# Kernel tuning notes

Measured on AMD Instinct MI355X. Metric: run time of the kernel, lower is better.

## Reference

```python
import jax, jax.numpy as jnp
import numpy as np

B, S, D, H = 4, 2048, 1024, 16
DH = D // H  # 64


def setup_inputs() -> dict:
    key = jax.random.key(0)
    ks = jax.random.split(key, 9)
    s_in = 1.0 / np.sqrt(D)
    inp = {
        "x_input": jax.random.normal(ks[0], (B, S, D), dtype=jnp.float32),
        # torch nn.Linear weights are [out, in]; y = x @ W.T + b
        "wq": jax.random.normal(ks[1], (D, D), dtype=jnp.float32) * s_in,
        "bq": jax.random.normal(ks[2], (D,), dtype=jnp.float32) * 0.01,
        "wk": jax.random.normal(ks[3], (D, D), dtype=jnp.float32) * s_in,
        "bk": jax.random.normal(ks[4], (D,), dtype=jnp.float32) * 0.01,
        "wv": jax.random.normal(ks[5], (D, D), dtype=jnp.float32) * s_in,
        "bv": jax.random.normal(ks[6], (D,), dtype=jnp.float32) * 0.01,
        "wo": jax.random.normal(ks[7], (D, D), dtype=jnp.float32) * s_in,
        "bo": jax.random.normal(ks[8], (D,), dtype=jnp.float32) * 0.01,
    }
    return inp


def reference(x_input, wq, bq, wk, bk, wv, bv, wo, bo):
    scale = 1.0 / np.sqrt(DH)
    q = x_input @ wq.T + bq  # [B,S,D]
    k = x_input @ wk.T + bk
    v = x_input @ wv.T + bv
    # split heads: [B,S,H,DH]
    q = q.reshape(B, S, H, DH)
    k = k.reshape(B, S, H, DH)
    v = v.reshape(B, S, H, DH)
    # scores [B,H,Sq,Sk] (vectorized over heads; same math as per-head loop)
    scores = jnp.einsum('bqhd,bkhd->bhqk', q, k) * scale
    attn = jax.nn.softmax(scores, axis=-1)
    out = jnp.einsum('bhqk,bkhd->bqhd', attn, v).reshape(B, S, D)
    return out @ wo.T + bo
```

## Files before the change

kernel.cpp:

```cpp
#include <hip/hip_runtime.h>

typedef unsigned short u16;
typedef unsigned int u32;
typedef unsigned int u32x2 __attribute__((ext_vector_type(2)));
typedef short bf16x8 __attribute__((ext_vector_type(8)));
typedef float f32x2 __attribute__((ext_vector_type(2)));
typedef float f32x4 __attribute__((ext_vector_type(4)));
typedef float f32x16 __attribute__((ext_vector_type(16)));

__device__ __forceinline__ u16 f2bf(float f) {
  unsigned int u = __builtin_bit_cast(unsigned int, f);
  u += 0x7FFFu + ((u >> 16) & 1u);
  return (u16)(u >> 16);
}

__device__ __forceinline__ u32 cvtpk(float lo, float hi) {
  u32 r;
  asm("v_cvt_pk_bf16_f32 %0, %1, %2" : "=v"(r) : "v"(lo), "v"(hi));
  return r;
}

#if __has_builtin(__builtin_amdgcn_exp2f)
#define EX2(x) __builtin_amdgcn_exp2f(x)
#else
extern "C" __device__ float __ocml_native_exp2_f32(float);
#define EX2(x) __ocml_native_exp2_f32(x)
#endif

#define MFMA16(a, b, c) __builtin_amdgcn_mfma_f32_16x16x32_bf16((a), (b), (c), 0, 0, 0)
#define MFMA32(a, b, c) __builtin_amdgcn_mfma_f32_32x32x16_bf16((a), (b), (c), 0, 0, 0)

#define GLL16(gp, lp) __builtin_amdgcn_global_load_lds( \
    (const __attribute__((address_space(1))) unsigned int*)(gp), \
    (__attribute__((address_space(3))) unsigned int*)(lp), 16, 0, 0)

__global__ __launch_bounds__(256) void cvt_bf16(const float* __restrict__ in,
                                                u16* __restrict__ out, int n4) {
  int i = blockIdx.x * 256 + threadIdx.x;
  const int stride = gridDim.x * 256;
  for (; i < n4; i += stride) {
    float4 f = ((const float4*)in)[i];
    u32x2 o;
    o[0] = cvtpk(f.x, f.y);
    o[1] = cvtpk(f.z, f.w);
    ((u32x2*)out)[i] = o;
  }
}

__global__ __launch_bounds__(256) void cvt_w4(const float* __restrict__ w0,
                                              const float* __restrict__ w1,
                                              const float* __restrict__ w2,
                                              const float* __restrict__ w3,
                                              u16* __restrict__ out) {
  const int wsel = blockIdx.y;
  const float* in = wsel == 0 ? w0 : wsel == 1 ? w1 : wsel == 2 ? w2 : w3;
  const int i = blockIdx.x * 256 + threadIdx.x;
  float4 f = ((const float4*)in)[i];
  u32x2 o;
  o[0] = cvtpk(f.x, f.y);
  o[1] = cvtpk(f.z, f.w);
  ((u32x2*)(out + (size_t)wsel * 1048576))[i] = o;
}

__global__ __launch_bounds__(256) void gemm_qkv(const u16* __restrict__ A,
                                                const u16* __restrict__ W,
                                                const float* __restrict__ bq,
                                                const float* __restrict__ bk,
                                                const float* __restrict__ bv,
                                                float qscale,
                                                u16* __restrict__ Qo,
                                                u16* __restrict__ Ko,
                                                u16* __restrict__ Vo) {
  __shared__ u16 As[128 * 64];
  __shared__ u16 Bs[128 * 64];
  const int t = threadIdx.x;
  const int wave = t >> 6, lane = t & 63;
  const int wg = blockIdx.x;
  const int s = (wg & 7) * 192 + (wg >> 3);
  const int bx = s & 63, by = s >> 6;
  const int bm = bx * 128, bn3 = by * 128;
  const int wr = (wave >> 1) * 64;
  const int wc = (wave & 1) * 64;
  f32x4 acc[4][4] = {};

  const u16* Ag[4];
  const u16* Bg[4];
#pragma unroll
  for (int i = 0; i < 4; i++) {
    const int c = i * 256 + t;
    const int row = c >> 3;
    const int g8 = (((c & 7) ^ (row & 7)) << 3);
    Ag[i] = A + (size_t)(bm + row) * 1024 + g8;
    Bg[i] = W + (size_t)(bn3 + row) * 1024 + g8;
  }

  const int frow = lane & 15;
  const int l4 = lane >> 4;

  for (int k0 = 0; k0 < 1024; k0 += 64) {
#pragma unroll
    for (int i = 0; i < 4; i++) GLL16(Ag[i], &As[i * 2048 + wave * 512]);
#pragma unroll
    for (int i = 0; i < 4; i++) GLL16(Bg[i], &Bs[i * 2048 + wave * 512]);
    __syncthreads();
    bf16x8 a[4][2], b[4][2];
#pragma unroll
    for (int m = 0; m < 4; m++) {
      const int row = wr + m * 16 + frow, sw = row & 7;
      a[m][0] = *(const bf16x8*)&As[row * 64 + ((l4 ^ sw) << 3)];
      a[m][1] = *(const bf16x8*)&As[row * 64 + (((l4 + 4) ^ sw) << 3)];
    }
#pragma unroll
    for (int n = 0; n < 4; n++) {
      const int row = wc + n * 16 + frow, sw = row & 7;
      b[n][0] = *(const bf16x8*)&Bs[row * 64 + ((l4 ^ sw) << 3)];
      b[n][1] = *(const bf16x8*)&Bs[row * 64 + (((l4 + 4) ^ sw) << 3)];
    }
#pragma unroll
    for (int m = 0; m < 4; m++)
#pragma unroll
      for (int n = 0; n < 4; n++) {
        acc[m][n] = MFMA16(a[m][0], b[n][0], acc[m][n]);
        acc[m][n] = MFMA16(a[m][1], b[n][1], acc[m][n]);
      }
    __syncthreads();
#pragma unroll
    for (int i = 0; i < 4; i++) { Ag[i] += 64; Bg[i] += 64; }
  }

  const int mode = by >> 3;
  const float* bias = mode == 0 ? bq : mode == 1 ? bk : bv;
  u16* out = mode == 0 ? Qo : Ko;
  const float alpha = mode == 0 ? qscale : 1.0f;

  const int crow0 = bm + wr + ((lane >> 4) << 2);
  const int ccolb = (bn3 & 1023) + wc + frow;
#pragma unroll
  for (int n = 0; n < 4; n++) {
    const int col = ccolb + n * 16;
    const float bvv = bias[col];
#pragma unroll
    for (int m = 0; m < 4; m++) {
      if (mode == 2) {
        const int row = crow0 + m * 16;
        u32x2 w;
        w[0] = cvtpk(acc[m][n][0] + bvv, acc[m][n][1] + bvv);
        w[1] = cvtpk(acc[m][n][2] + bvv, acc[m][n][3] + bvv);
        size_t off = ((size_t)((row >> 11) * 16 + (col >> 6)) * 64 + (col & 63)) * 2048 + (row & 2047);
        *(u32x2*)(Vo + off) = w;
      } else {
#pragma unroll
        for (int r = 0; r < 4; r++) {
          float v = (acc[m][n][r] + bvv) * alpha;
          out[(size_t)(crow0 + m * 16 + r) * 1024 + col] = f2bf(v);
        }
      }
    }
  }
}

__global__ __launch_bounds__(256) void gemm_out(const u16* __restrict__ A,
                                                const u16* __restrict__ W,
                                                const float* __restrict__ bias,
                                                float* __restrict__ C) {
  __shared__ u16 As[128 * 64];
  __shared__ u16 Bs[128 * 64];
  const int t = threadIdx.x;
  const int wave = t >> 6, lane = t & 63;
  const int wg = blockIdx.x;
  const int s = (wg & 7) * 64 + (wg >> 3);
  const int bx = s & 63, by = s >> 6;
  const int bm = bx * 128, bn = by * 128;
  const int wr = (wave >> 1) * 64;
  const int wc = (wave & 1) * 64;
  f32x4 acc[4][4] = {};

  const u16* Ag[4];
  const u16* Bg[4];
#pragma unroll
  for (int i = 0; i < 4; i++) {
    const int c = i * 256 + t;
    const int row = c >> 3;
    const int g8 = (((c & 7) ^ (row & 7)) << 3);
    Ag[i] = A + (size_t)(bm + row) * 1024 + g8;
    Bg[i] = W + (size_t)(bn + row) * 1024 + g8;
  }

  const int frow = lane & 15;
  const int l4 = lane >> 4;

  for (int k0 = 0; k0 < 1024; k0 += 64) {
#pragma unroll
    for (int i = 0; i < 4; i++) GLL16(Ag[i], &As[i * 2048 + wave * 512]);
#pragma unroll
    for (int i = 0; i < 4; i++) GLL16(Bg[i], &Bs[i * 2048 + wave * 512]);
    __syncthreads();
    bf16x8 a[4][2], b[4][2];
#pragma unroll
    for (int m = 0; m < 4; m++) {
      const int row = wr + m * 16 + frow, sw = row & 7;
      a[m][0] = *(const bf16x8*)&As[row * 64 + ((l4 ^ sw) << 3)];
      a[m][1] = *(const bf16x8*)&As[row * 64 + (((l4 + 4) ^ sw) << 3)];
    }
#pragma unroll
    for (int n = 0; n < 4; n++) {
      const int row = wc + n * 16 + frow, sw = row & 7;
      b[n][0] = *(const bf16x8*)&Bs[row * 64 + ((l4 ^ sw) << 3)];
      b[n][1] = *(const bf16x8*)&Bs[row * 64 + (((l4 + 4) ^ sw) << 3)];
    }
#pragma unroll
    for (int m = 0; m < 4; m++)
#pragma unroll
      for (int n = 0; n < 4; n++) {
        acc[m][n] = MFMA16(a[m][0], b[n][0], acc[m][n]);
        acc[m][n] = MFMA16(a[m][1], b[n][1], acc[m][n]);
      }
    __syncthreads();
#pragma unroll
    for (int i = 0; i < 4; i++) { Ag[i] += 64; Bg[i] += 64; }
  }

  const int crow0 = bm + wr + ((lane >> 4) << 2);
  const int ccol = bn + wc + frow;
#pragma unroll
  for (int n = 0; n < 4; n++) {
    float bvv = bias[ccol + n * 16];
#pragma unroll
    for (int m = 0; m < 4; m++)
#pragma unroll
      for (int r = 0; r < 4; r++)
        C[(size_t)(crow0 + m * 16 + r) * 1024 + (ccol + n * 16)] = acc[m][n][r] + bvv;
  }
}

__global__ __launch_bounds__(256, 4) void attn2(const u16* __restrict__ Q,
                                                const u16* __restrict__ K,
                                                const u16* __restrict__ VT,
                                                u16* __restrict__ O) {
  __shared__ u16 ks[2][4096];
  __shared__ u16 vs[4096];
  __shared__ u16 ps[4][2048];
  const int t = threadIdx.x;
  const int lane = t & 63, warp = t >> 6;
  const int g = lane >> 5, ql = lane & 31;
  const int wg = blockIdx.x;
  const int idx = wg >> 3;
  const int bh = ((wg & 7) << 3) + (idx >> 4);
  const int qblk = idx & 15;
  const int b = bh >> 4, h = bh & 15;

  bf16x8 qf[4];
  {
    const u16* qp = Q + (size_t)(b * 2048 + qblk * 128 + warp * 32 + ql) * 1024 + h * 64 + 8 * g;
#pragma unroll
    for (int kk = 0; kk < 4; kk++) qf[kk] = *(const bf16x8*)(qp + 16 * kk);
  }

  int offRC[2][4];
#pragma unroll
  for (int kk = 0; kk < 4; kk++) {
    int x = (((2 * kk + g) ^ (ql & 7)) << 3);
    offRC[0][kk] = ql * 64 + x;
    offRC[1][kk] = (32 + ql) * 64 + x;
  }

  const int c0 = t, c1 = t + 256;
  const int r0 = c0 >> 3, r1 = c1 >> 3;
  const u16* kp0 = K + (size_t)(b * 2048 + r0) * 1024 + h * 64 + (((c0 & 7) ^ (r0 & 7)) << 3);
  const u16* kp1 = K + (size_t)(b * 2048 + r1) * 1024 + h * 64 + (((c1 & 7) ^ (r1 & 7)) << 3);
  const u16* vp0 = VT + ((size_t)bh * 64 + r0) * 2048 + (((c0 & 7) ^ (r0 & 7)) << 3);
  const u16* vp1 = VT + ((size_t)bh * 64 + r1) * 2048 + (((c1 & 7) ^ (r1 & 7)) << 3);
  const size_t kadv = (size_t)64 * 1024;

  f32x16 o0 = {}, o1 = {};
  float l = 0.f;

  GLL16(kp0, &ks[0][warp * 512]);
  GLL16(kp1, &ks[0][2048 + warp * 512]);
  kp0 += kadv; kp1 += kadv;
  __syncthreads();

  u16* pwq = &ps[warp][0] + ql * 64;
  const int sw = ql & 7;
  const int e4 = (((ql >> 3) ^ (ql >> 4)) & 1) << 2;

  int cur = 0;
  for (int kt = 0; kt < 32; kt++) {
    const int nxt = cur ^ 1;
    GLL16(vp0, &vs[warp * 512]);
    GLL16(vp1, &vs[2048 + warp * 512]);
    vp0 += 64; vp1 += 64;
    GLL16(kp0, &ks[nxt][warp * 512]);
    GLL16(kp1, &ks[nxt][2048 + warp * 512]);
    kp0 += kadv; kp1 += kadv;

    const u16* kb = ks[cur];

    f32x16 s0 = {}, s1 = {};
    __builtin_amdgcn_s_setprio(1);
#pragma unroll
    for (int kk = 0; kk < 4; kk++) {
      bf16x8 ka = *(const bf16x8*)(kb + offRC[0][kk]);
      bf16x8 kc = *(const bf16x8*)(kb + offRC[1][kk]);
      s0 = MFMA32(ka, qf[kk], s0);
      s1 = MFMA32(kc, qf[kk], s1);
    }
    __builtin_amdgcn_s_setprio(0);

    {
      f32x2* s0p = (f32x2*)&s0;
      f32x2* s1p = (f32x2*)&s1;
      f32x2 tsum[8];
#pragma unroll
      for (int i = 0; i < 8; i++) {
        f32x2 d0 = s0p[i], d1 = s1p[i];
        d0[0] = EX2(d0[0]); d0[1] = EX2(d0[1]);
        d1[0] = EX2(d1[0]); d1[1] = EX2(d1[1]);
        s0p[i] = d0; s1p[i] = d1;
        tsum[i] = d0 + d1;
      }
#pragma unroll
      for (int i = 0; i < 4; i++) tsum[i] += tsum[i + 4];
      tsum[0] += tsum[2]; tsum[1] += tsum[3];
      tsum[0] += tsum[1];
      l += tsum[0][0] + tsum[0][1];
    }

#pragma unroll
    for (int q4 = 0; q4 < 4; q4++) {
      u32x2 wa, wb;
      wa[0] = cvtpk(s0[4 * q4 + 0], s0[4 * q4 + 1]);
      wa[1] = cvtpk(s0[4 * q4 + 2], s0[4 * q4 + 3]);
      wb[0] = cvtpk(s1[4 * q4 + 0], s1[4 * q4 + 1]);
      wb[1] = cvtpk(s1[4 * q4 + 2], s1[4 * q4 + 3]);
      const int so = (g << 2) ^ e4;
      *(u32x2*)(pwq + ((q4 ^ sw) << 3) + so) = wa;
      *(u32x2*)(pwq + (((q4 + 4) ^ sw) << 3) + so) = wb;
    }
    asm volatile("s_waitcnt lgkmcnt(0)" ::: "memory");
    __builtin_amdgcn_sched_barrier(0);

    bf16x8 pf[4];
#pragma unroll
    for (int kg = 0; kg < 4; kg++) {
      const u16* gb = pwq + (((2 * kg + g) ^ sw) << 3);
      union { u32x2 w[2]; bf16x8 v; } u;
      u.w[0] = *(const u32x2*)(gb + e4);
      u.w[1] = *(const u32x2*)(gb + (e4 ^ 4));
      pf[kg] = u.v;
    }

    asm volatile("s_waitcnt vmcnt(2)" ::: "memory");
    __builtin_amdgcn_s_barrier();
    __builtin_amdgcn_sched_barrier(0);

    __builtin_amdgcn_s_setprio(1);
#pragma unroll
    for (int kg = 0; kg < 4; kg++) {
      bf16x8 va = *(const bf16x8*)(vs + offRC[0][kg]);
      bf16x8 vc = *(const bf16x8*)(vs + offRC[1][kg]);
      o0 = MFMA32(va, pf[kg], o0);
      o1 = MFMA32(vc, pf[kg], o1);
    }
    __builtin_amdgcn_s_setprio(0);

    asm volatile("s_waitcnt vmcnt(0)" ::: "memory");
    __builtin_amdgcn_s_barrier();
    __builtin_amdgcn_sched_barrier(0);
    cur = nxt;
  }

  l += __shfl_xor(l, 32);
  const float rinv = 1.0f / l;
  u16* op = O + (size_t)(b * 2048 + qblk * 128 + warp * 32 + ql) * 1024 + h * 64;
#pragma unroll
  for (int half = 0; half < 2; half++) {
    const f32x16& oo = half ? o1 : o0;
#pragma unroll
    for (int p = 0; p < 4; p++) {
      u32x2 w;
      w[0] = cvtpk(oo[4 * p + 0] * rinv, oo[4 * p + 1] * rinv);
      w[1] = cvtpk(oo[4 * p + 2] * rinv, oo[4 * p + 3] * rinv);
      const int dh = 8 * p + 4 * g + 32 * half;
      *(u32x2*)(op + dh) = w;
    }
  }
}

extern "C" void kernel_launch(void* const* d_in, const int* in_sizes, int n_in,
                              void* d_out, int out_size, void* d_ws, size_t ws_size,
                              hipStream_t stream) {
  const float* x  = (const float*)d_in[0];
  const float* wq = (const float*)d_in[1];
  const float* bq = (const float*)d_in[2];
  const float* wk = (const float*)d_in[3];
  const float* bk = (const float*)d_in[4];
  const float* wv = (const float*)d_in[5];
  const float* bv = (const float*)d_in[6];
  const float* wo = (const float*)d_in[7];
  const float* bo = (const float*)d_in[8];

  u16* xb  = (u16*)d_ws;
  u16* wqb = xb + 8388608;
  u16* wob = wqb + 3145728;
  u16* qb  = wob + 1048576;
  u16* kb  = qb + 8388608;
  u16* vtb = kb + 8388608;
  u16* ob  = xb;

  cvt_bf16<<<2048, 256, 0, stream>>>(x, xb, 8388608 / 4);
  cvt_w4<<<dim3(1024, 4), 256, 0, stream>>>(wq, wk, wv, wo, wqb);

  const float qscale = 0.125f * 1.44269504088896f;
  gemm_qkv<<<1536, 256, 0, stream>>>(xb, wqb, bq, bk, bv, qscale, qb, kb, vtb);

  attn2<<<1024, 256, 0, stream>>>(qb, kb, vtb, ob);

  gemm_out<<<512, 256, 0, stream>>>(ob, wob, bo, (float*)d_out);
}
```

Before: 206.0 us.

## Process two query sub-tiles per warp in attention to reuse K/V tiles

Each attention workgroup now handles 256 query rows instead of 128: every warp computes two 32-row query slices against the same K and V tiles held in shared memory. This halves the grid and halves the global K/V traffic and the LDS K/V reads per query row. In exchange it doubles the accumulator and fragment registers per thread, lowers the launch-bounds occupancy hint from 4 to 2, and leaves fewer workgroups to fill the GPU.

```diff
diff --git a/kernel.cpp b/kernel.cpp
--- a/kernel.cpp
+++ b/kernel.cpp
@@ -233,7 +233,7 @@
   }
 }
 
-__global__ __launch_bounds__(256, 4) void attn2(const u16* __restrict__ Q,
+__global__ __launch_bounds__(256, 2) void attn2(const u16* __restrict__ Q,
                                                 const u16* __restrict__ K,
                                                 const u16* __restrict__ VT,
                                                 u16* __restrict__ O) {
@@ -245,15 +245,16 @@
   const int g = lane >> 5, ql = lane & 31;
   const int wg = blockIdx.x;
   const int idx = wg >> 3;
-  const int bh = ((wg & 7) << 3) + (idx >> 4);
-  const int qblk = idx & 15;
+  const int bh = ((wg & 7) << 3) + (idx >> 3);
+  const int qblk = idx & 7;
   const int b = bh >> 4, h = bh & 15;
 
-  bf16x8 qf[4];
-  {
-    const u16* qp = Q + (size_t)(b * 2048 + qblk * 128 + warp * 32 + ql) * 1024 + h * 64 + 8 * g;
-#pragma unroll
-    for (int kk = 0; kk < 4; kk++) qf[kk] = *(const bf16x8*)(qp + 16 * kk);
+  bf16x8 qf[2][4];
+#pragma unroll
+  for (int s = 0; s < 2; s++) {
+    const u16* qp = Q + (size_t)(b * 2048 + qblk * 256 + warp * 64 + s * 32 + ql) * 1024 + h * 64 + 8 * g;
+#pragma unroll
+    for (int kk = 0; kk < 4; kk++) qf[s][kk] = *(const bf16x8*)(qp + 16 * kk);
   }
 
   int offRC[2][4];
@@ -272,8 +273,8 @@
   const u16* vp1 = VT + ((size_t)bh * 64 + r1) * 2048 + (((c1 & 7) ^ (r1 & 7)) << 3);
   const size_t kadv = (size_t)64 * 1024;
 
-  f32x16 o0 = {}, o1 = {};
-  float l = 0.f;
+  f32x16 oa0 = {}, oa1 = {}, ob0 = {}, ob1 = {};
+  float l0 = 0.f, l1 = 0.f;
 
   GLL16(kp0, &ks[0][warp * 512]);
   GLL16(kp1, &ks[0][2048 + warp * 512]);
@@ -283,6 +284,7 @@
   u16* pwq = &ps[warp][0] + ql * 64;
   const int sw = ql & 7;
   const int e4 = (((ql >> 3) ^ (ql >> 4)) & 1) << 2;
+  const int so = (g << 2) ^ e4;
 
   int cur = 0;
   for (int kt = 0; kt < 32; kt++) {
@@ -296,58 +298,69 @@
 
     const u16* kb = ks[cur];
 
-    f32x16 s0 = {}, s1 = {};
-    __builtin_amdgcn_s_setprio(1);
+    bf16x8 kf0[4], kf1[4];
 #pragma unroll
     for (int kk = 0; kk < 4; kk++) {
-      bf16x8 ka = *(const bf16x8*)(kb + offRC[0][kk]);
-      bf16x8 kc = *(const bf16x8*)(kb + offRC[1][kk]);
-      s0 = MFMA32(ka, qf[kk], s0);
-      s1 = MFMA32(kc, qf[kk], s1);
-    }
-    __builtin_amdgcn_s_setprio(0);
-
-    {
-      f32x2* s0p = (f32x2*)&s0;
-      f32x2* s1p = (f32x2*)&s1;
-      f32x2 tsum[8];
-#pragma unroll
-      for (int i = 0; i < 8; i++) {
-        f32x2 d0 = s0p[i], d1 = s1p[i];
-        d0[0] = EX2(d0[0]); d0[1] = EX2(d0[1]);
-        d1[0] = EX2(d1[0]); d1[1] = EX2(d1[1]);
-        s0p[i] = d0; s1p[i] = d1;
-        tsum[i] = d0 + d1;
-      }
-#pragma unroll
-      for (int i = 0; i < 4; i++) tsum[i] += tsum[i + 4];
-      tsum[0] += tsum[2]; tsum[1] += tsum[3];
-      tsum[0] += tsum[1];
-      l += tsum[0][0] + tsum[0][1];
-    }
-
-#pragma unroll
-    for (int q4 = 0; q4 < 4; q4++) {
-      u32x2 wa, wb;
-      wa[0] = cvtpk(s0[4 * q4 + 0], s0[4 * q4 + 1]);
-      wa[1] = cvtpk(s0[4 * q4 + 2], s0[4 * q4 + 3]);
-      wb[0] = cvtpk(s1[4 * q4 + 0], s1[4 * q4 + 1]);
-      wb[1] = cvtpk(s1[4 * q4 + 2], s1[4 * q4 + 3]);
-      const int so = (g << 2) ^ e4;
-      *(u32x2*)(pwq + ((q4 ^ sw) << 3) + so) = wa;
-      *(u32x2*)(pwq + (((q4 + 4) ^ sw) << 3) + so) = wb;
-    }
-    asm volatile("s_waitcnt lgkmcnt(0)" ::: "memory");
-    __builtin_amdgcn_sched_barrier(0);
-
-    bf16x8 pf[4];
-#pragma unroll
-    for (int kg = 0; kg < 4; kg++) {
-      const u16* gb = pwq + (((2 * kg + g) ^ sw) << 3);
-      union { u32x2 w[2]; bf16x8 v; } u;
-      u.w[0] = *(const u32x2*)(gb + e4);
-      u.w[1] = *(const u32x2*)(gb + (e4 ^ 4));
-      pf[kg] = u.v;
+      kf0[kk] = *(const bf16x8*)(kb + offRC[0][kk]);
+      kf1[kk] = *(const bf16x8*)(kb + offRC[1][kk]);
+    }
+
+    bf16x8 pf0[4], pf1[4];
+#pragma unroll
+    for (int s = 0; s < 2; s++) {
+      f32x16 s0 = {}, s1 = {};
+      __builtin_amdgcn_s_setprio(1);
+#pragma unroll
+      for (int kk = 0; kk < 4; kk++) {
+        s0 = MFMA32(kf0[kk], qf[s][kk], s0);
+        s1 = MFMA32(kf1[kk], qf[s][kk], s1);
+      }
+      __builtin_amdgcn_s_setprio(0);
+
+      {
+        f32x2* s0p = (f32x2*)&s0;
+        f32x2* s1p = (f32x2*)&s1;
+        f32x2 tsum[8];
+#pragma unroll
+        for (int i = 0; i < 8; i++) {
+          f32x2 d0 = s0p[i], d1 = s1p[i];
+          d0[0] = EX2(d0[0]); d0[1] = EX2(d0[1]);
+          d1[0] = EX2(d1[0]); d1[1] = EX2(d1[1]);
+          s0p[i] = d0; s1p[i] = d1;
+          tsum[i] = d0 + d1;
+        }
+#pragma unroll
+        for (int i = 0; i < 4; i++) tsum[i] += tsum[i + 4];
+        tsum[0] += tsum[2]; tsum[1] += tsum[3];
+        tsum[0] += tsum[1];
+        if (s == 0) l0 += tsum[0][0] + tsum[0][1];
+        else        l1 += tsum[0][0] + tsum[0][1];
+      }
+
+#pragma unroll
+      for (int q4 = 0; q4 < 4; q4++) {
+        u32x2 wa, wb;
+        wa[0] = cvtpk(s0[4 * q4 + 0], s0[4 * q4 + 1]);
+        wa[1] = cvtpk(s0[4 * q4 + 2], s0[4 * q4 + 3]);
+        wb[0] = cvtpk(s1[4 * q4 + 0], s1[4 * q4 + 1]);
+        wb[1] = cvtpk(s1[4 * q4 + 2], s1[4 * q4 + 3]);
+        *(u32x2*)(pwq + ((q4 ^ sw) << 3) + so) = wa;
+        *(u32x2*)(pwq + (((q4 + 4) ^ sw) << 3) + so) = wb;
+      }
+      asm volatile("s_waitcnt lgkmcnt(0)" ::: "memory");
+      __builtin_amdgcn_sched_barrier(0);
+
+      bf16x8* pf = s == 0 ? pf0 : pf1;
+#pragma unroll
+      for (int kg = 0; kg < 4; kg++) {
+        const u16* gb = pwq + (((2 * kg + g) ^ sw) << 3);
+        union { u32x2 w[2]; bf16x8 v; } u;
+        u.w[0] = *(const u32x2*)(gb + e4);
+        u.w[1] = *(const u32x2*)(gb + (e4 ^ 4));
+        pf[kg] = u.v;
+      }
+      asm volatile("s_waitcnt lgkmcnt(0)" ::: "memory");
+      __builtin_amdgcn_sched_barrier(0);
     }
 
     asm volatile("s_waitcnt vmcnt(2)" ::: "memory");
@@ -359,8 +372,10 @@
     for (int kg = 0; kg < 4; kg++) {
       bf16x8 va = *(const bf16x8*)(vs + offRC[0][kg]);
       bf16x8 vc = *(const bf16x8*)(vs + offRC[1][kg]);
-      o0 = MFMA32(va, pf[kg], o0);
-      o1 = MFMA32(vc, pf[kg], o1);
+      oa0 = MFMA32(va, pf0[kg], oa0);
+      oa1 = MFMA32(vc, pf0[kg], oa1);
+      ob0 = MFMA32(va, pf1[kg], ob0);
+      ob1 = MFMA32(vc, pf1[kg], ob1);
     }
     __builtin_amdgcn_s_setprio(0);
 
@@ -370,19 +385,23 @@
     cur = nxt;
   }
 
-  l += __shfl_xor(l, 32);
-  const float rinv = 1.0f / l;
-  u16* op = O + (size_t)(b * 2048 + qblk * 128 + warp * 32 + ql) * 1024 + h * 64;
-#pragma unroll
-  for (int half = 0; half < 2; half++) {
-    const f32x16& oo = half ? o1 : o0;
-#pragma unroll
-    for (int p = 0; p < 4; p++) {
-      u32x2 w;
-      w[0] = cvtpk(oo[4 * p + 0] * rinv, oo[4 * p + 1] * rinv);
-      w[1] = cvtpk(oo[4 * p + 2] * rinv, oo[4 * p + 3] * rinv);
-      const int dh = 8 * p + 4 * g + 32 * half;
-      *(u32x2*)(op + dh) = w;
+  l0 += __shfl_xor(l0, 32);
+  l1 += __shfl_xor(l1, 32);
+#pragma unroll
+  for (int s = 0; s < 2; s++) {
+    const float rinv = 1.0f / (s == 0 ? l0 : l1);
+    u16* op = O + (size_t)(b * 2048 + qblk * 256 + warp * 64 + s * 32 + ql) * 1024 + h * 64;
+#pragma unroll
+    for (int half = 0; half < 2; half++) {
+      const f32x16& oo = s == 0 ? (half ? oa1 : oa0) : (half ? ob1 : ob0);
+#pragma unroll
+      for (int p = 0; p < 4; p++) {
+        u32x2 w;
+        w[0] = cvtpk(oo[4 * p + 0] * rinv, oo[4 * p + 1] * rinv);
+        w[1] = cvtpk(oo[4 * p + 2] * rinv, oo[4 * p + 3] * rinv);
+        const int dh = 8 * p + 4 * g + 32 * half;
+        *(u32x2*)(op + dh) = w;
+      }
     }
   }
 }
@@ -414,7 +433,7 @@
   const float qscale = 0.125f * 1.44269504088896f;
   gemm_qkv<<<1536, 256, 0, stream>>>(xb, wqb, bq, bk, bv, qscale, qb, kb, vtb);
 
-  attn2<<<1024, 256, 0, stream>>>(qb, kb, vtb, ob);
+  attn2<<<512, 256, 0, stream>>>(qb, kb, vtb, ob);
 
   gemm_out<<<512, 256, 0, stream>>>(ob, wob, bo, (float*)d_out);
 }
```

Measured after the change: 203.2 us. About the same (-1.3%).
